# Kernel optimization log

Measured on AMD Instinct MI355X. Metric: run time of the kernel, lower is better.

Reference implementation:

```python
import jax, jax.numpy as jnp
import numpy as np

RADIUS = 2
SIGMA_SPATIAL = 2.5
SIGMA_RANGE_FACTOR = 0.5


def setup_inputs() -> dict:
    key = jax.random.key(0)
    k1, k2 = jax.random.split(key)
    source = jax.random.normal(k1, (4, 64, 64, 64), dtype=jnp.float32)
    guidance = jax.random.uniform(k2, (4, 3, 256, 256), dtype=jnp.float32)
    return {"source": source, "guidance": guidance}


def _jbu(source, guidance):
    # source: [B, C, h, w] low-res features; guidance: [B, Cg, H, W] high-res image
    B, C, h, w = source.shape
    _, Cg, H, W = guidance.shape
    s = H // h  # integer upsampling factor
    r = RADIUS

    # per-batch range sigma from guidance std (torch.std is unbiased -> ddof=1)
    sigma_range = SIGMA_RANGE_FACTOR * jnp.std(guidance, axis=(1, 2, 3), ddof=1)  # [B]
    inv_2sr2 = 1.0 / (2.0 * sigma_range * sigma_range)  # [B]
    inv_2ss2 = 1.0 / (2.0 * SIGMA_SPATIAL * SIGMA_SPATIAL)

    # guidance sampled at low-res cell centers: [B, Cg, h, w]
    off = s // 2
    g_low = guidance[:, :, off::s, off::s]

    # low-res center index for every hi-res pixel
    yc = jnp.arange(H) // s  # [H]
    xc = jnp.arange(W) // s  # [W]

    num = jnp.zeros((B, C, H, W), dtype=source.dtype)
    den = jnp.zeros((B, 1, H, W), dtype=source.dtype)

    # fixed small (2r+1)^2 = 25 window taps; unrolled loop, each tap is a
    # clamped gather + fused weight compute + accumulate (no huge intermediates)
    for dy in range(-r, r + 1):
        yi = jnp.clip(yc + dy, 0, h - 1)  # [H]
        for dx in range(-r, r + 1):
            xi = jnp.clip(xc + dx, 0, w - 1)  # [W]
            src_g = source[:, :, yi[:, None], xi[None, :]]  # [B, C, H, W]
            g_g = g_low[:, :, yi[:, None], xi[None, :]]      # [B, Cg, H, W]
            diff2 = jnp.sum((guidance - g_g) ** 2, axis=1)   # [B, H, W]
            w_range = jnp.exp(-diff2 * inv_2sr2[:, None, None])
            w_spatial = np.exp(-(dy * dy + dx * dx) * 1.0) ** 0.0  # placeholder removed below
            w_spatial = jnp.exp(jnp.asarray(-(dy * dy + dx * dx) * inv_2ss2, dtype=source.dtype))
            wgt = (w_spatial * w_range)[:, None]  # [B, 1, H, W]
            num = num + src_g * wgt
            den = den + wgt

    return num / (den + 1e-8)


def reference(source, guidance):
    return _jbu(source, guidance)
```

## Files before the change

### kernel.cpp

```cpp
#include <hip/hip_runtime.h>

#define B_  4
#define C_  64
#define H_  256
#define W_  256
#define h_  64
#define w_  64
#define L2SW2 (-0.46166241f)
#define L2SW1 (-0.11541560f)

typedef float v2f __attribute__((ext_vector_type(2)));

__global__ void jbu_stats(const float* __restrict__ g, double* __restrict__ stats) {
    int b     = blockIdx.x >> 3;
    int slice = blockIdx.x & 7;
    const float4* p = (const float4*)(g + (size_t)b * 3 * H_ * W_) + (size_t)slice * 6144;
    double s = 0.0, s2 = 0.0;
    for (int i = threadIdx.x; i < 6144; i += 256) {
        float4 v = p[i];
        s  += (double)v.x + (double)v.y + (double)v.z + (double)v.w;
        s2 += (double)v.x * v.x + (double)v.y * v.y
            + (double)v.z * v.z + (double)v.w * v.w;
    }
    for (int off = 32; off > 0; off >>= 1) {
        s  += __shfl_down(s,  off);
        s2 += __shfl_down(s2, off);
    }
    __shared__ double ls[8];
    int wid  = threadIdx.x >> 6;
    int lane = threadIdx.x & 63;
    if (lane == 0) { ls[wid] = s; ls[4 + wid] = s2; }
    __syncthreads();
    if (threadIdx.x == 0) {
        stats[blockIdx.x]      = ls[0] + ls[1] + ls[2] + ls[3];
        stats[32 + blockIdx.x] = ls[4] + ls[5] + ls[6] + ls[7];
    }
}

__global__ __launch_bounds__(256, 4)
void jbu_mega16(const float* __restrict__ src, const float* __restrict__ guid,
                const double* __restrict__ stats, float* __restrict__ out) {
    __shared__ __align__(16) float sS[5 * 64 * 20];
    __shared__ __align__(16) float sG[5 * 64 * 4];

    int cg  = blockIdx.x & 3;
    int y4  = (blockIdx.x >> 2) & 63;
    int b   = blockIdx.x >> 8;
    int tid = threadIdx.x;

    int yi[5];
    #pragma unroll
    for (int d = 0; d < 5; ++d) {
        int u = y4 + d - 2;
        yi[d] = u < 0 ? 0 : (u > h_ - 1 ? h_ - 1 : u);
    }

    const float* sb = src + ((size_t)b * C_ + cg * 16) * h_ * w_;
    {
        int xx0 = tid & 63;
        int j4  = ((tid >> 6) & 3) * 4;
        #pragma unroll
        for (int it = 0; it < 5; ++it) {
            int yy = yi[it];
            float4 v;
            v.x = sb[((size_t)(j4 + 0) * h_ + yy) * w_ + xx0];
            v.y = sb[((size_t)(j4 + 1) * h_ + yy) * w_ + xx0];
            v.z = sb[((size_t)(j4 + 2) * h_ + yy) * w_ + xx0];
            v.w = sb[((size_t)(j4 + 3) * h_ + yy) * w_ + xx0];
            *(float4*)&sS[(it * 64 + xx0) * 20 + j4] = v;
        }
    }
    for (int k = tid; k < 320; k += 256) {
        int xx  = k & 63;
        int row = k >> 6;
        int u   = y4 + row - 2;
        int yy  = u < 0 ? 0 : (u > h_ - 1 ? h_ - 1 : u);
        const float* gbase = guid + (size_t)b * 3 * H_ * W_
                           + (size_t)(yy * 4 + 2) * W_ + (xx * 4 + 2);
        float gx = gbase[0];
        float gy = gbase[H_ * W_];
        float gz = gbase[2 * H_ * W_];
        float ss = fmaf(gz, gz, fmaf(gy, gy, gx * gx));
        float4 e = make_float4(gx, gy, gz, ss);
        *(float4*)&sG[(row * 64 + xx) * 4] = e;
    }

    double S = 0.0, S2 = 0.0;
    for (int i = 0; i < 8; ++i) {
        S  += stats[b * 8 + i];
        S2 += stats[32 + b * 8 + i];
    }
    const double n = 3.0 * H_ * W_;
    double var = (S2 - S * S / n) / (n - 1.0);
    float invrl2 = (float)(2.0 / var) * 1.44269504f;
    float ninv   = -invrl2;

    int x  = tid;
    int y0 = y4 * 4;
    float gp[4][3];
    float A[4];
    #pragma unroll
    for (int c = 0; c < 3; ++c)
        #pragma unroll
        for (int p = 0; p < 4; ++p)
            gp[p][c] = guid[(((size_t)b * 3 + c) * H_ + (y0 + p)) * W_ + x];
    float t2 = 2.0f * invrl2;
    #pragma unroll
    for (int p = 0; p < 4; ++p) {
        float ss = fmaf(gp[p][2], gp[p][2], fmaf(gp[p][1], gp[p][1], gp[p][0] * gp[p][0]));
        A[p] = -invrl2 * ss;
        gp[p][0] *= t2; gp[p][1] *= t2; gp[p][2] *= t2;
    }

    __syncthreads();

    int xb = x >> 2;
    int xi[5];
    #pragma unroll
    for (int d = 0; d < 5; ++d) {
        int v = xb + d - 2;
        xi[d] = v < 0 ? 0 : (v > w_ - 1 ? w_ - 1 : v);
    }

    const float l2sw[5] = {L2SW2, L2SW1, 0.0f, L2SW1, L2SW2};

    v2f accv[4][8];
    float den[4];
    #pragma unroll
    for (int p = 0; p < 4; ++p) {
        den[p] = 0.0f;
        #pragma unroll
        for (int j = 0; j < 8; ++j) { accv[p][j].x = 0.0f; accv[p][j].y = 0.0f; }
    }

    #pragma unroll
    for (int dy = 0; dy < 5; ++dy) {
        float l2y = l2sw[dy];
        int   rb  = dy * 64;
        #pragma unroll
        for (int dx = 0; dx < 5; ++dx) {
            int xx = xi[dx];
            float4 gl = *(const float4*)&sG[(rb + xx) * 4];
            float ct = fmaf(gl.w, ninv, l2y + l2sw[dx]);
            v2f w2[4];
            #pragma unroll
            for (int p = 0; p < 4; ++p) {
                float m = fmaf(gp[p][2], gl.z,
                          fmaf(gp[p][1], gl.y,
                          fmaf(gp[p][0], gl.x, ct + A[p])));
                float wv = __builtin_amdgcn_exp2f(m);
                w2[p].x = wv; w2[p].y = wv;
                den[p] += wv;
            }
            const float* sP = &sS[(rb + xx) * 20];
            #pragma unroll
            for (int q = 0; q < 4; ++q) {
                v2f lo = *(const v2f*)(sP + q * 4);
                v2f hi = *(const v2f*)(sP + q * 4 + 2);
                #pragma unroll
                for (int p = 0; p < 4; ++p) {
                    asm("v_pk_fma_f32 %0, %1, %2, %0"
                        : "+v"(accv[p][q * 2 + 0]) : "v"(w2[p]), "v"(lo));
                    asm("v_pk_fma_f32 %0, %1, %2, %0"
                        : "+v"(accv[p][q * 2 + 1]) : "v"(w2[p]), "v"(hi));
                }
            }
        }
    }

    float* ob = out + ((size_t)b * C_ + cg * 16) * H_ * W_;
    #pragma unroll
    for (int p = 0; p < 4; ++p) {
        float r = 1.0f / (den[p] + 1e-8f);
        int row = (y0 + p) * W_ + x;
        #pragma unroll
        for (int j = 0; j < 8; ++j) {
            __builtin_nontemporal_store(accv[p][j].x * r, &ob[(size_t)(2 * j + 0) * H_ * W_ + row]);
            __builtin_nontemporal_store(accv[p][j].y * r, &ob[(size_t)(2 * j + 1) * H_ * W_ + row]);
        }
    }
}

extern "C" void kernel_launch(void* const* d_in, const int* in_sizes, int n_in,
                              void* d_out, int out_size, void* d_ws, size_t ws_size,
                              hipStream_t stream) {
    const float* src  = (const float*)d_in[0];
    const float* guid = (const float*)d_in[1];
    float* out = (float*)d_out;

    double* stats = (double*)d_ws;

    jbu_stats<<<32, 256, 0, stream>>>(guid, stats);
    jbu_mega16<<<B_ * 64 * 4, 256, 0, stream>>>(src, guid, stats, out);
}
```

Before: 98.13 us.

## Split each row-block into four 64-pixel x-quarters with single-wavefront blocks

Changes the main kernel from 256-thread blocks covering a full 256-pixel row strip to 64-thread (one wavefront) blocks covering a 64-pixel quarter, giving four times as many blocks. Each block now stages only a 20-column low-res halo window (100 cells) of source and guidance into shared memory instead of full 64-column rows. This cuts LDS per block and removes clamped x-index arithmetic in the inner loop. The cost is redundant halo loads across neighbouring quarters, more block launches, and each block's staging being done by a single wavefront.

```diff
diff --git a/kernel.cpp b/kernel.cpp
--- a/kernel.cpp
+++ b/kernel.cpp
@@ -37,52 +37,57 @@
     }
 }
 
-__global__ __launch_bounds__(256, 4)
-void jbu_mega16(const float* __restrict__ src, const float* __restrict__ guid,
-                const double* __restrict__ stats, float* __restrict__ out) {
-    __shared__ __align__(16) float sS[5 * 64 * 20];
-    __shared__ __align__(16) float sG[5 * 64 * 4];
+__global__ __launch_bounds__(64, 4)
+void jbu_quar(const float* __restrict__ src, const float* __restrict__ guid,
+              const double* __restrict__ stats, float* __restrict__ out) {
+    __shared__ __align__(16) float sS[100 * 20];
+    __shared__ __align__(16) float sG[100 * 4];
 
-    int cg  = blockIdx.x & 3;
-    int y4  = (blockIdx.x >> 2) & 63;
-    int b   = blockIdx.x >> 8;
+    int xh  = blockIdx.x & 3;
+    int cg  = (blockIdx.x >> 2) & 3;
+    int y4  = (blockIdx.x >> 4) & 63;
+    int b   = blockIdx.x >> 10;
     int tid = threadIdx.x;
 
-    int yi[5];
-    #pragma unroll
-    for (int d = 0; d < 5; ++d) {
-        int u = y4 + d - 2;
-        yi[d] = u < 0 ? 0 : (u > h_ - 1 ? h_ - 1 : u);
-    }
+    int gc0 = xh * 16 - 2;
 
     const float* sb = src + ((size_t)b * C_ + cg * 16) * h_ * w_;
-    {
-        int xx0 = tid & 63;
-        int j4  = ((tid >> 6) & 3) * 4;
-        #pragma unroll
-        for (int it = 0; it < 5; ++it) {
-            int yy = yi[it];
+    #pragma unroll
+    for (int it = 0; it < 7; ++it) {
+        int k = it * 64 + tid;
+        if (k < 400) {
+            int quad = k & 3;
+            int cell = k >> 2;
+            int row  = cell / 20;
+            int l    = cell - row * 20;
+            int gc   = gc0 + l;  gc = gc < 0 ? 0 : (gc > w_ - 1 ? w_ - 1 : gc);
+            int yy   = y4 + row - 2; yy = yy < 0 ? 0 : (yy > h_ - 1 ? h_ - 1 : yy);
+            int j4   = quad * 4;
             float4 v;
-            v.x = sb[((size_t)(j4 + 0) * h_ + yy) * w_ + xx0];
-            v.y = sb[((size_t)(j4 + 1) * h_ + yy) * w_ + xx0];
-            v.z = sb[((size_t)(j4 + 2) * h_ + yy) * w_ + xx0];
-            v.w = sb[((size_t)(j4 + 3) * h_ + yy) * w_ + xx0];
-            *(float4*)&sS[(it * 64 + xx0) * 20 + j4] = v;
+            v.x = sb[((size_t)(j4 + 0) * h_ + yy) * w_ + gc];
+            v.y = sb[((size_t)(j4 + 1) * h_ + yy) * w_ + gc];
+            v.z = sb[((size_t)(j4 + 2) * h_ + yy) * w_ + gc];
+            v.w = sb[((size_t)(j4 + 3) * h_ + yy) * w_ + gc];
+            *(float4*)&sS[cell * 20 + j4] = v;
         }
     }
-    for (int k = tid; k < 320; k += 256) {
-        int xx  = k & 63;
-        int row = k >> 6;
-        int u   = y4 + row - 2;
-        int yy  = u < 0 ? 0 : (u > h_ - 1 ? h_ - 1 : u);
-        const float* gbase = guid + (size_t)b * 3 * H_ * W_
-                           + (size_t)(yy * 4 + 2) * W_ + (xx * 4 + 2);
-        float gx = gbase[0];
-        float gy = gbase[H_ * W_];
-        float gz = gbase[2 * H_ * W_];
-        float ss = fmaf(gz, gz, fmaf(gy, gy, gx * gx));
-        float4 e = make_float4(gx, gy, gz, ss);
-        *(float4*)&sG[(row * 64 + xx) * 4] = e;
+    #pragma unroll
+    for (int it = 0; it < 2; ++it) {
+        int k = it * 64 + tid;
+        if (k < 100) {
+            int row = k / 20;
+            int l   = k - row * 20;
+            int gc  = gc0 + l;  gc = gc < 0 ? 0 : (gc > w_ - 1 ? w_ - 1 : gc);
+            int yy  = y4 + row - 2; yy = yy < 0 ? 0 : (yy > h_ - 1 ? h_ - 1 : yy);
+            const float* gbase = guid + (size_t)b * 3 * H_ * W_
+                               + (size_t)(yy * 4 + 2) * W_ + (gc * 4 + 2);
+            float gx = gbase[0];
+            float gy = gbase[H_ * W_];
+            float gz = gbase[2 * H_ * W_];
+            float ss = fmaf(gz, gz, fmaf(gy, gy, gx * gx));
+            float4 e = make_float4(gx, gy, gz, ss);
+            *(float4*)&sG[k * 4] = e;
+        }
     }
 
     double S = 0.0, S2 = 0.0;
@@ -95,7 +100,7 @@
     float invrl2 = (float)(2.0 / var) * 1.44269504f;
     float ninv   = -invrl2;
 
-    int x  = tid;
+    int xg = xh * 64 + tid;
     int y0 = y4 * 4;
     float gp[4][3];
     float A[4];
@@ -103,7 +108,7 @@
     for (int c = 0; c < 3; ++c)
         #pragma unroll
         for (int p = 0; p < 4; ++p)
-            gp[p][c] = guid[(((size_t)b * 3 + c) * H_ + (y0 + p)) * W_ + x];
+            gp[p][c] = guid[(((size_t)b * 3 + c) * H_ + (y0 + p)) * W_ + xg];
     float t2 = 2.0f * invrl2;
     #pragma unroll
     for (int p = 0; p < 4; ++p) {
@@ -114,13 +119,7 @@
 
     __syncthreads();
 
-    int xb = x >> 2;
-    int xi[5];
-    #pragma unroll
-    for (int d = 0; d < 5; ++d) {
-        int v = xb + d - 2;
-        xi[d] = v < 0 ? 0 : (v > w_ - 1 ? w_ - 1 : v);
-    }
+    int xbl = tid >> 2;
 
     const float l2sw[5] = {L2SW2, L2SW1, 0.0f, L2SW1, L2SW2};
 
@@ -136,11 +135,11 @@
     #pragma unroll
     for (int dy = 0; dy < 5; ++dy) {
         float l2y = l2sw[dy];
-        int   rb  = dy * 64;
+        int   rb  = dy * 20 + xbl;
         #pragma unroll
         for (int dx = 0; dx < 5; ++dx) {
-            int xx = xi[dx];
-            float4 gl = *(const float4*)&sG[(rb + xx) * 4];
+            int cell = rb + dx;
+            float4 gl = *(const float4*)&sG[cell * 4];
             float ct = fmaf(gl.w, ninv, l2y + l2sw[dx]);
             v2f w2[4];
             #pragma unroll
@@ -152,7 +151,7 @@
                 w2[p].x = wv; w2[p].y = wv;
                 den[p] += wv;
             }
-            const float* sP = &sS[(rb + xx) * 20];
+            const float* sP = &sS[cell * 20];
             #pragma unroll
             for (int q = 0; q < 4; ++q) {
                 v2f lo = *(const v2f*)(sP + q * 4);
@@ -172,7 +171,7 @@
     #pragma unroll
     for (int p = 0; p < 4; ++p) {
         float r = 1.0f / (den[p] + 1e-8f);
-        int row = (y0 + p) * W_ + x;
+        int row = (y0 + p) * W_ + xg;
         #pragma unroll
         for (int j = 0; j < 8; ++j) {
             __builtin_nontemporal_store(accv[p][j].x * r, &ob[(size_t)(2 * j + 0) * H_ * W_ + row]);
@@ -191,5 +190,5 @@
     double* stats = (double*)d_ws;
 
     jbu_stats<<<32, 256, 0, stream>>>(guid, stats);
-    jbu_mega16<<<B_ * 64 * 4, 256, 0, stream>>>(src, guid, stats, out);
+    jbu_quar<<<B_ * 64 * 4 * 4, 64, 0, stream>>>(src, guid, stats, out);
 }
```

Measured after the change: 99.99 us. About the same (+1.9%).
